# Kernel optimization log

Hardware: AMD Instinct MI355X
Metric: run time of the kernel (lower is better)

The kernel has to match this reference:

```python
import jax, jax.numpy as jnp
import numpy as np

HEADS = 4
DIM_HEAD = 32  # total inner dim; per-head dim = DIM_HEAD // HEADS = 8
SCALE = DIM_HEAD ** -0.5  # faithful to original: scale uses dim_head, not per-head dim


def setup_inputs() -> dict:
    key = jax.random.key(0)
    k_x, k_q, k_kv, k_o, k_pe = jax.random.split(key, 5)
    B, L, dim = 131072, 4, 256
    inner = DIM_HEAD
    x = jax.random.normal(k_x, (B, L, dim), dtype=jnp.float32)
    Wq = jax.random.normal(k_q, (dim, inner), dtype=jnp.float32) * 0.02
    Wkv = jax.random.normal(k_kv, (dim, 2 * inner), dtype=jnp.float32) * 0.02
    Wo = jax.random.normal(k_o, (inner, dim), dtype=jnp.float32) * 0.02
    bo = jnp.zeros((dim,), dtype=jnp.float32)
    pos_emb = jax.random.normal(k_pe, (1, HEADS, L, L), dtype=jnp.float32)
    return {"x": x, "Wq": Wq, "Wkv": Wkv, "Wo": Wo, "bo": bo, "pos_emb": pos_emb}


def reference(x, Wq, Wkv, Wo, bo, pos_emb):
    B, L, dim = x.shape
    dh = DIM_HEAD // HEADS  # per-head dim
    q = x @ Wq                       # [B, L, inner]
    kv = x @ Wkv                     # [B, L, 2*inner]
    k, v = jnp.split(kv, 2, axis=-1)
    # [B, L, inner] -> [B, heads, L, dh]
    split_heads = lambda t: t.reshape(B, L, HEADS, dh).transpose(0, 2, 1, 3)
    q, k, v = map(split_heads, (q, k, v))
    q = q * SCALE
    sim = jnp.einsum('bhid,bhjd->bhij', q, k) + pos_emb  # [B, heads, L, L]
    attn = jax.nn.softmax(sim, axis=-1)
    out = jnp.einsum('bhij,bhjd->bhid', attn, v)         # [B, heads, L, dh]
    out = out.transpose(0, 2, 1, 3).reshape(B, L, HEADS * dh)
    return out @ Wo + bo             # [B, L, dim]
```

## Files before the change

kernel.cpp:

```cpp
#include <hip/hip_runtime.h>
#include <hip/hip_bf16.h>

typedef float  f32x4  __attribute__((ext_vector_type(4)));
typedef __bf16 bf16x8 __attribute__((ext_vector_type(8)));

#define SCALE_QK 0.17677669529663687f


template<int CTRL>
__device__ __forceinline__ float dpp_add(float x) {
  int xi = __builtin_bit_cast(int, x);
  int yi = __builtin_amdgcn_mov_dpp(xi, CTRL, 0xF, 0xF, true);
  return x + __builtin_bit_cast(float, yi);
}

__global__ void pack_weights(const float* __restrict__ Wq, const float* __restrict__ Wkv,
                             const float* __restrict__ Wo, __bf16* __restrict__ wsf) {
  const int item = blockIdx.x * 256 + threadIdx.x;
  const int f = item >> 6, lane = item & 63;
  const int g = lane >> 4, c = lane & 15;
  union { bf16x8 v; __bf16 h[8]; } vv;
  if (f < 48) {
    const int kt = f / 6, ct = f - kt * 6;
    const int n = ct * 16 + c;
    #pragma unroll
    for (int j = 0; j < 8; ++j) {
      const int k = kt * 32 + g * 8 + j;
      vv.h[j] = (__bf16)((n < 32) ? Wq[k * 32 + n] : Wkv[k * 64 + (n - 32)]);
    }
  } else {
    const int ct = f - 48;
    const int n = ct * 16 + c;
    #pragma unroll
    for (int j = 0; j < 8; ++j) vv.h[j] = (__bf16)Wo[(g * 8 + j) * 256 + n];
  }
  *(bf16x8*)&wsf[item * 8] = vv.v;
}

#define FR1(f) (*(const bf16x8*)&wfrag1[(f) * 512 + lane * 8])
#define MFMA(a, b, cc) __builtin_amdgcn_mfma_f32_16x16x32_bf16((a), (b), (cc), 0, 0, 0)

#define LDS_TOTAL 154112

__global__ __launch_bounds__(192, 1) void fused_stattn(
    const float* __restrict__ x, const __bf16* __restrict__ wsf,
    const float* __restrict__ bo, const float* __restrict__ pe,
    float* __restrict__ out) {
  extern __shared__ char smem[];

  const int tid  = threadIdx.x;
  const int lane = tid & 63;
  const int wv   = tid >> 6;
  const int g    = lane >> 4;
  const int c    = lane & 15;

  __bf16* wfrag1 = (__bf16*)smem;
  char*   stg0   = smem + 49152 + wv * 33280;
  __bf16* aoW    = (__bf16*)(smem + 148992 + wv * 1280);
  float*  bo_l   = (float*)(smem + 152832);
  float*  pe_l   = (float*)(smem + 153856);

  bf16x8 wo[16];
  #pragma unroll
  for (int i = 0; i < 16; ++i)
    wo[i] = *(const bf16x8*)&wsf[((48 + i) * 64 + lane) * 8];

  #pragma unroll
  for (int it = 0; it < 16; ++it) {
    const int idx = it * 192 + tid;
    *(bf16x8*)&wfrag1[idx * 8] = *(const bf16x8*)&wsf[idx * 8];
  }
  bo_l[tid] = bo[tid];
  if (tid < 64) bo_l[192 + tid] = bo[192 + tid];
  if (tid < 64) pe_l[tid] = pe[tid];
  __syncthreads();

  const unsigned stg_lds = (unsigned)(unsigned long long)(void*)stg0;

  auto stage_tile = [&](unsigned dbase, int tile) {
    const float* src = x + (size_t)tile * 4096 + (lane << 2);
    #pragma unroll
    for (int r = 0; r < 16; ++r) {
      __builtin_amdgcn_global_load_lds(
          (const __attribute__((address_space(1))) void*)(src + r * 256),
          (__attribute__((address_space(3))) void*)(unsigned long long)(dbase + r * 1040),
          16, 0, 0);
    }
  };

  const int slot = blockIdx.x * 3 + wv;
  int cur = 0;
  stage_tile(stg_lds, slot);

  for (int tile = slot; tile < 32768; tile += 3072) {
    const int nt = tile + 3072;
    asm volatile("s_waitcnt lgkmcnt(0)" ::: "memory");
    if (nt < 32768) stage_tile(stg_lds + (unsigned)((cur ^ 1) * 16640), nt);
    asm volatile("s_waitcnt vmcnt(16)" ::: "memory");
    __builtin_amdgcn_sched_barrier(0);

    char* stg = stg0 + cur * 16640;

    f32x4 acc0 = {0,0,0,0}, acc1 = {0,0,0,0}, acc2 = {0,0,0,0};
    f32x4 acc3 = {0,0,0,0}, acc4 = {0,0,0,0}, acc5 = {0,0,0,0};
    #pragma unroll
    for (int kt = 0; kt < 8; ++kt) {
      const f32x4 va = *(const f32x4*)(stg + c * 1040 + kt * 128 + g * 32);
      const f32x4 vb = *(const f32x4*)(stg + c * 1040 + kt * 128 + g * 32 + 16);
      union { bf16x8 v; __bf16 h[8]; } af;
      #pragma unroll
      for (int j = 0; j < 4; ++j) { af.h[j] = (__bf16)va[j]; af.h[4+j] = (__bf16)vb[j]; }
      acc0 = MFMA(af.v, FR1(kt*6+0), acc0);
      acc1 = MFMA(af.v, FR1(kt*6+1), acc1);
      acc2 = MFMA(af.v, FR1(kt*6+2), acc2);
      acc3 = MFMA(af.v, FR1(kt*6+3), acc3);
      acc4 = MFMA(af.v, FR1(kt*6+4), acc4);
      acc5 = MFMA(af.v, FR1(kt*6+5), acc5);
    }

    const int h0 = c >> 3;
    float ao0[4], ao1[4];
    #pragma unroll
    for (int p = 0; p < 2; ++p) {
      const f32x4 qa = p ? acc1 : acc0;
      const f32x4 ka = p ? acc3 : acc2;
      const f32x4 va = p ? acc5 : acc4;
      const int ph = 2 * p + h0;
      float sim[4][4];
      #pragma unroll
      for (int i = 0; i < 4; ++i)
        #pragma unroll
        for (int j = 0; j < 4; ++j) {
          float pr = qa[i] * ka[j];
          pr = dpp_add<0xB1>(pr);
          pr = dpp_add<0x4E>(pr);
          pr = dpp_add<0x141>(pr);
          sim[i][j] = pr * SCALE_QK + pe_l[ph * 16 + i * 4 + j];
        }
      #pragma unroll
      for (int i = 0; i < 4; ++i) {
        const float m = fmaxf(fmaxf(sim[i][0], sim[i][1]), fmaxf(sim[i][2], sim[i][3]));
        const float e0 = __expf(sim[i][0] - m), e1 = __expf(sim[i][1] - m);
        const float e2 = __expf(sim[i][2] - m), e3 = __expf(sim[i][3] - m);
        const float rs = 1.0f / (e0 + e1 + e2 + e3);
        const float o  = (e0*va[0] + e1*va[1] + e2*va[2] + e3*va[3]) * rs;
        if (p) ao1[i] = o; else ao0[i] = o;
      }
    }

    #pragma unroll
    for (int i = 0; i < 4; ++i) {
      aoW[(g*4 + i) * 40 + c]      = (__bf16)ao0[i];
      aoW[(g*4 + i) * 40 + 16 + c] = (__bf16)ao1[i];
    }
    const bf16x8 a2 = *(const bf16x8*)&aoW[c * 40 + g * 8];

    #pragma unroll
    for (int ct = 0; ct < 16; ++ct) {
      const f32x4 bv = *(const f32x4*)&bo_l[ct * 16 + g * 4];
      f32x4 o = MFMA(wo[ct], a2, bv);
      *(f32x4*)(stg + c * 1040 + ct * 64 + g * 16) = o;
    }

    {
      float* orow = out + (size_t)tile * 4096 + (lane << 2);
      #pragma unroll
      for (int r = 0; r < 16; ++r) {
        const f32x4 v = *(const f32x4*)(stg + r * 1040 + lane * 16);
        *(f32x4*)(orow + r * 256) = v;
      }
    }

    cur ^= 1;
  }
}

extern "C" void kernel_launch(void* const* d_in, const int* in_sizes, int n_in,
                              void* d_out, int out_size, void* d_ws, size_t ws_size,
                              hipStream_t stream) {
  const float* x   = (const float*)d_in[0];
  const float* Wq  = (const float*)d_in[1];
  const float* Wkv = (const float*)d_in[2];
  const float* Wo  = (const float*)d_in[3];
  const float* bo  = (const float*)d_in[4];
  const float* pe  = (const float*)d_in[5];
  float* out = (float*)d_out;
  __bf16* wsf = (__bf16*)d_ws;

  (void)hipFuncSetAttribute(reinterpret_cast<const void*>(fused_stattn),
                            hipFuncAttributeMaxDynamicSharedMemorySize, LDS_TOTAL);
  hipLaunchKernelGGL(pack_weights, dim3(16), dim3(256), 0, stream, Wq, Wkv, Wo, wsf);
  hipLaunchKernelGGL(fused_stattn, dim3(1024), dim3(192), LDS_TOTAL, stream,
                     x, wsf, bo, pe, out);
}
```

Baseline: 214.2 us.

## Keep half the QKV weight fragments in registers and run four waves per block

Moves 25 of the 48 QKV weight fragments from LDS into VGPRs, which frees LDS for a fourth wave's double-buffered staging area, and raises the block size from 192 to 256 threads. Tiles are now assigned as contiguous runs of 8 per wave instead of a strided loop. The aim is to cut LDS weight reads in the projection loop and add more waves to hide memory latency. The cost is much higher register pressure (wo plus wfr use about 164 VGPRs), which risks spilling.

```diff
diff --git a/kernel.cpp b/kernel.cpp
--- a/kernel.cpp
+++ b/kernel.cpp
@@ -37,12 +37,15 @@
   *(bf16x8*)&wsf[item * 8] = vv.v;
 }
 
-#define FR1(f) (*(const bf16x8*)&wfrag1[(f) * 512 + lane * 8])
 #define MFMA(a, b, cc) __builtin_amdgcn_mfma_f32_16x16x32_bf16((a), (b), (cc), 0, 0, 0)
-
-#define LDS_TOTAL 154112
-
-__global__ __launch_bounds__(192, 1) void fused_stattn(
+#define VMW(n) do { asm volatile("s_waitcnt vmcnt(" #n ")" ::: "memory"); \
+                    __builtin_amdgcn_sched_barrier(0); } while (0)
+#define WF(f) (((f) < 25) ? wfr[(f) % 25] \
+                          : (*(const bf16x8*)&wfragL[(((f) < 25) ? 0 : (f) - 25) * 512 + lane * 8]))
+
+#define LDS_TOTAL 163072
+
+__global__ __launch_bounds__(256, 1) void fused_stattn(
     const float* __restrict__ x, const __bf16* __restrict__ wsf,
     const float* __restrict__ bo, const float* __restrict__ pe,
     float* __restrict__ out) {
@@ -54,25 +57,34 @@
   const int g    = lane >> 4;
   const int c    = lane & 15;
 
-  __bf16* wfrag1 = (__bf16*)smem;
-  char*   stg0   = smem + 49152 + wv * 33280;
-  __bf16* aoW    = (__bf16*)(smem + 148992 + wv * 1280);
-  float*  bo_l   = (float*)(smem + 152832);
-  float*  pe_l   = (float*)(smem + 153856);
+  __bf16* wfragL = (__bf16*)smem;
+  char*   stg0   = smem + 23552 + wv * 33280;
+  __bf16* aoW    = (__bf16*)(smem + 156672 + wv * 1280);
+  float*  bo_l   = (float*)(smem + 161792);
+  float*  pe_l   = (float*)(smem + 162816);
 
   bf16x8 wo[16];
   #pragma unroll
   for (int i = 0; i < 16; ++i)
     wo[i] = *(const bf16x8*)&wsf[((48 + i) * 64 + lane) * 8];
-
-  #pragma unroll
-  for (int it = 0; it < 16; ++it) {
-    const int idx = it * 192 + tid;
-    *(bf16x8*)&wfrag1[idx * 8] = *(const bf16x8*)&wsf[idx * 8];
+  bf16x8 wfr[25];
+  #pragma unroll
+  for (int i = 0; i < 25; ++i)
+    wfr[i] = *(const bf16x8*)&wsf[(i * 64 + lane) * 8];
+
+  #pragma unroll
+  for (int it = 0; it < 6; ++it) {
+    const int idx = it * 256 + tid;
+    if (idx < 1472)
+      *(bf16x8*)&wfragL[idx * 8] = *(const bf16x8*)&wsf[(1600 + idx) * 8];
   }
   bo_l[tid] = bo[tid];
-  if (tid < 64) bo_l[192 + tid] = bo[192 + tid];
   if (tid < 64) pe_l[tid] = pe[tid];
+
+  #pragma unroll
+  for (int i = 0; i < 16; ++i) asm volatile("" :: "v"(wo[i]));
+  #pragma unroll
+  for (int i = 0; i < 25; ++i) asm volatile("" :: "v"(wfr[i]));
   __syncthreads();
 
   const unsigned stg_lds = (unsigned)(unsigned long long)(void*)stg0;
@@ -88,16 +100,17 @@
     }
   };
 
-  const int slot = blockIdx.x * 3 + wv;
+  const int slot  = blockIdx.x * 4 + wv;
+  const int tile0 = slot * 8;
+
   int cur = 0;
-  stage_tile(stg_lds, slot);
-
-  for (int tile = slot; tile < 32768; tile += 3072) {
-    const int nt = tile + 3072;
+  stage_tile(stg_lds, tile0);
+
+  for (int t = 0; t < 8; ++t) {
+    const int tile = tile0 + t;
     asm volatile("s_waitcnt lgkmcnt(0)" ::: "memory");
-    if (nt < 32768) stage_tile(stg_lds + (unsigned)((cur ^ 1) * 16640), nt);
-    asm volatile("s_waitcnt vmcnt(16)" ::: "memory");
-    __builtin_amdgcn_sched_barrier(0);
+    if (t < 7) stage_tile(stg_lds + (unsigned)((cur ^ 1) * 16640), tile + 1);
+    VMW(16);
 
     char* stg = stg0 + cur * 16640;
 
@@ -110,12 +123,12 @@
       union { bf16x8 v; __bf16 h[8]; } af;
       #pragma unroll
       for (int j = 0; j < 4; ++j) { af.h[j] = (__bf16)va[j]; af.h[4+j] = (__bf16)vb[j]; }
-      acc0 = MFMA(af.v, FR1(kt*6+0), acc0);
-      acc1 = MFMA(af.v, FR1(kt*6+1), acc1);
-      acc2 = MFMA(af.v, FR1(kt*6+2), acc2);
-      acc3 = MFMA(af.v, FR1(kt*6+3), acc3);
-      acc4 = MFMA(af.v, FR1(kt*6+4), acc4);
-      acc5 = MFMA(af.v, FR1(kt*6+5), acc5);
+      acc0 = MFMA(af.v, WF(kt*6+0), acc0);
+      acc1 = MFMA(af.v, WF(kt*6+1), acc1);
+      acc2 = MFMA(af.v, WF(kt*6+2), acc2);
+      acc3 = MFMA(af.v, WF(kt*6+3), acc3);
+      acc4 = MFMA(af.v, WF(kt*6+4), acc4);
+      acc5 = MFMA(af.v, WF(kt*6+5), acc5);
     }
 
     const int h0 = c >> 3;
@@ -190,6 +203,6 @@
   (void)hipFuncSetAttribute(reinterpret_cast<const void*>(fused_stattn),
                             hipFuncAttributeMaxDynamicSharedMemorySize, LDS_TOTAL);
   hipLaunchKernelGGL(pack_weights, dim3(16), dim3(256), 0, stream, Wq, Wkv, Wo, wsf);
-  hipLaunchKernelGGL(fused_stattn, dim3(1024), dim3(192), LDS_TOTAL, stream,
+  hipLaunchKernelGGL(fused_stattn, dim3(1024), dim3(256), LDS_TOTAL, stream,
                      x, wsf, bo, pe, out);
 }
```

New measurement: 241.9 us. +12.9%, slower.
